# Kernel tuning notes

Hardware: AMD Instinct MI355X
Metric: run time of the kernel (lower is better)

## Reference

```python
import jax, jax.numpy as jnp
import numpy as np

NFFT = 4_194_304
NMODES = 2
NTAPS = 101
GAMMA = 0.0016567  # [/W/m]
DZ = 80000.0       # [m]


def setup_inputs() -> dict:
    key = jax.random.key(0)
    k1, k2, k3 = jax.random.split(key, 3)
    xr = jax.random.normal(k1, (NFFT, NMODES), dtype=jnp.float32)
    xi = jax.random.normal(k2, (NFFT, NMODES), dtype=jnp.float32)
    # fconv1d kernel: [ntaps, in_features=Nmodes, out_features=Nmodes] (lecun_normal-ish scale)
    W = jax.random.normal(k3, (NTAPS, NMODES, NMODES), dtype=jnp.float32) / np.sqrt(NTAPS * NMODES)
    b = jnp.zeros((NMODES,), dtype=jnp.float32)
    power = jnp.zeros((1,), dtype=jnp.float32)  # 0 dBm
    return {"xr": xr, "xi": xi, "W": W, "b": b, "power": power}


def reference(xr, xi, W, b, power):
    # P = |x|^2, shape [Nfft, Nmodes]
    P = xr * xr + xi * xi
    # valid 1D conv over time: [Nfft, Nmodes] -> [Nfft - ntaps + 1, Nmodes]
    phi = jax.lax.conv_general_dilated(
        P[None],            # [1, Nfft, Nmodes]
        W,                  # [ntaps, in, out]
        window_strides=(1,),
        padding='VALID',
        dimension_numbers=('NWC', 'WIO', 'NWC'),
    )[0] + b                # [Nfft - ntaps + 1, Nmodes]

    nmodes = xr.shape[-1]
    scale = 0.001 * 10.0 ** (power[0] / 10.0) / nmodes  # dBm -> W, per mode
    n0 = NTAPS // 2
    x = (xr + 1j * xi)[n0:xr.shape[0] - n0]  # valid-conv aligned slice
    y = x * jnp.exp(-1j * phi * (GAMMA * scale * DZ))
    return y
```

## Files before the change

### kernel.cpp

```cpp
#include <hip/hip_runtime.h>
#include <hip/hip_bf16.h>

#define NFFT   4194304
#define NMODES 2
#define NTAPS  101
#define NVALID (NFFT - NTAPS + 1)
#define N0     (NTAPS / 2)

constexpr int BLOCK = 256;
constexpr int CPT   = 8;
constexpr int TILE  = BLOCK * CPT;
constexpr int WIN   = TILE + NTAPS - 1;
constexpr int PITCH = 269;

static __device__ __forceinline__ unsigned short f2bf(float x) {
    __hip_bfloat16 h = __float2bfloat16(x);
    return *reinterpret_cast<unsigned short*>(&h);
}
static __device__ __forceinline__ unsigned pk(float e0, float e1) {
    return (unsigned)f2bf(e0) | ((unsigned)f2bf(e1) << 16);
}

__global__ __launch_bounds__(BLOCK, 4) void nl_kernel(
    const float* __restrict__ xa,
    const float* __restrict__ xb,
    const float* __restrict__ W,  const float* __restrict__ b,
    const float* __restrict__ power, unsigned* __restrict__ out)
{
    __shared__ float2 Pl[CPT * PITCH];

    const int tid = threadIdx.x;
    const int tile_start = blockIdx.x * TILE;

    const float2* __restrict__ xa2 = reinterpret_cast<const float2*>(xa);
    const float2* __restrict__ xb2 = reinterpret_cast<const float2*>(xb);
    for (int idx = tid; idx < WIN; idx += BLOCK) {
        const int g = tile_start + idx;
        float2 p = make_float2(0.f, 0.f);
        if (g < NFFT) {
            const float2 a = xa2[g];
            const float2 c = xb2[g];
            p.x = a.x * a.x + c.x * c.x;
            p.y = a.y * a.y + c.y * c.y;
        }
        Pl[(idx & 7) * PITCH + (idx >> 3)] = p;
    }
    __syncthreads();

    float acc[CPT][2];
    const float b0 = b[0], b1 = b[1];
    #pragma unroll
    for (int c = 0; c < CPT; ++c) { acc[c][0] = b0; acc[c][1] = b1; }

    const float4* __restrict__ W4 = reinterpret_cast<const float4*>(W);

    float2 w[16];
    #pragma unroll
    for (int m = 0; m < 15; ++m)
        w[m] = Pl[(m & 7) * PITCH + tid + (m >> 3)];

    for (int K = 0; K < 6; ++K) {
        const int krow = tid + 2 * K;
        #pragma unroll
        for (int j = 0; j < 16; ++j) {
            w[(j + 15) & 15] = Pl[((j + 7) & 7) * PITCH + krow + ((j + 15) >> 3)];
            const float4 wt = W4[16 * K + j];
            #pragma unroll
            for (int c = 0; c < CPT; ++c) {
                const float2 p = w[(j + c) & 15];
                acc[c][0] = fmaf(p.x, wt.x, fmaf(p.y, wt.z, acc[c][0]));
                acc[c][1] = fmaf(p.x, wt.y, fmaf(p.y, wt.w, acc[c][1]));
            }
        }
    }
    #pragma unroll
    for (int j = 0; j < 5; ++j) {
        const float4 wt = W4[96 + j];
        #pragma unroll
        for (int c = 0; c < CPT; ++c) {
            const float2 p = w[(96 + j + c) & 15];
            acc[c][0] = fmaf(p.x, wt.x, fmaf(p.y, wt.z, acc[c][0]));
            acc[c][1] = fmaf(p.x, wt.y, fmaf(p.y, wt.w, acc[c][1]));
        }
    }

    const float coef = 0.066268f * exp10f(power[0] * 0.1f);
    const int base = tile_start + tid * CPT;

    const float4* __restrict__ xa4 = reinterpret_cast<const float4*>(xa);
    const float4* __restrict__ xb4 = reinterpret_cast<const float4*>(xb);
    uint4* __restrict__ out4 = reinterpret_cast<uint4*>(out);

    #pragma unroll
    for (int cc = 0; cc < 4; ++cc) {
        const int n0 = base + 2 * cc;
        const int c0 = 2 * cc;
        if (n0 + 1 < NVALID) {
            const float4 A = xa4[(n0 + N0) >> 1];
            const float4 B = xb4[(n0 + N0) >> 1];
            float s00, c00, s01, c01, s10, c10, s11, c11;
            __sincosf(acc[c0][0]     * coef, &s00, &c00);
            __sincosf(acc[c0][1]     * coef, &s01, &c01);
            __sincosf(acc[c0 + 1][0] * coef, &s10, &c10);
            __sincosf(acc[c0 + 1][1] * coef, &s11, &c11);
            uint4 o;
            o.x = pk(B.x * c00 - A.x * s00, A.x * c00 + B.x * s00);
            o.y = pk(B.y * c01 - A.y * s01, A.y * c01 + B.y * s01);
            o.z = pk(B.z * c10 - A.z * s10, A.z * c10 + B.z * s10);
            o.w = pk(B.w * c11 - A.w * s11, A.w * c11 + B.w * s11);
            out4[n0 >> 1] = o;
        } else {
            #pragma unroll
            for (int dc = 0; dc < 2; ++dc) {
                const int n = n0 + dc;
                if (n < NVALID) {
                    const float2 A = xa2[n + N0];
                    const float2 B = xb2[n + N0];
                    float s0, c0s, s1, c1s;
                    __sincosf(acc[c0 + dc][0] * coef, &s0, &c0s);
                    __sincosf(acc[c0 + dc][1] * coef, &s1, &c1s);
                    uint2 o;
                    o.x = pk(B.x * c0s - A.x * s0, A.x * c0s + B.x * s0);
                    o.y = pk(B.y * c1s - A.y * s1, A.y * c1s + B.y * s1);
                    reinterpret_cast<uint2*>(out)[n] = o;
                }
            }
        }
    }
}

extern "C" void kernel_launch(void* const* d_in, const int* in_sizes, int n_in,
                              void* d_out, int out_size, void* d_ws, size_t ws_size,
                              hipStream_t stream) {
    const float* big[2] = {nullptr, nullptr};
    const float* W = nullptr; const float* b = nullptr; const float* power = nullptr;
    int nbig = 0;
    for (int i = 0; i < n_in; ++i) {
        const float* p = (const float*)d_in[i];
        const int sz = in_sizes[i];
        if (sz == NFFT * NMODES)       { if (nbig < 2) big[nbig++] = p; }
        else if (sz == NTAPS * NMODES * NMODES) { W = p; }
        else if (sz == NMODES)         { b = p; }
        else if (sz == 1)              { power = p; }
    }

    unsigned* out = (unsigned*)d_out;
    const int grid = (NVALID + TILE - 1) / TILE;
    nl_kernel<<<grid, BLOCK, 0, stream>>>(big[0], big[1], W, b, power, out);
}
```

Before: 137.5 us.

## Compute 101-tap convolution with bf16 MFMA using Toeplitz weight fragments in a persistent grid

```diff
diff --git a/kernel.cpp b/kernel.cpp
--- a/kernel.cpp
+++ b/kernel.cpp
@@ -8,10 +8,14 @@
 #define N0     (NTAPS / 2)
 
 constexpr int BLOCK = 256;
-constexpr int CPT   = 8;
-constexpr int TILE  = BLOCK * CPT;
-constexpr int WIN   = TILE + NTAPS - 1;
-constexpr int PITCH = 269;
+constexpr int TILE  = 2048;
+constexpr int NT    = (NVALID + TILE - 1) / TILE;
+constexpr int GRID  = 1024;
+constexpr int WIN   = 2176;
+constexpr int NM    = 15;
+
+typedef __attribute__((ext_vector_type(8)))  short short8;
+typedef __attribute__((ext_vector_type(16))) float float16;
 
 static __device__ __forceinline__ unsigned short f2bf(float x) {
     __hip_bfloat16 h = __float2bfloat16(x);
@@ -20,110 +24,101 @@
 static __device__ __forceinline__ unsigned pk(float e0, float e1) {
     return (unsigned)f2bf(e0) | ((unsigned)f2bf(e1) << 16);
 }
+static __device__ __forceinline__ int swz(int s) {
+    return s ^ (((s >> 5) & 7) << 2);
+}
 
-__global__ __launch_bounds__(BLOCK, 4) void nl_kernel(
+__global__ __launch_bounds__(BLOCK, 3) void nl_kernel(
     const float* __restrict__ xa,
     const float* __restrict__ xb,
     const float* __restrict__ W,  const float* __restrict__ b,
     const float* __restrict__ power, unsigned* __restrict__ out)
 {
-    __shared__ float2 Pl[CPT * PITCH];
+    __shared__ __align__(16) unsigned Pl[WIN];
 
-    const int tid = threadIdx.x;
-    const int tile_start = blockIdx.x * TILE;
+    const int tid  = threadIdx.x;
+    const int lane = tid & 63;
+    const int wid  = tid >> 6;
+    const int colc = lane & 31;
+    const int h    = lane >> 5;
+    const int cs   = colc >> 1;
+    const int o    = colc & 1;
+    const int r    = colc;
 
-    const float2* __restrict__ xa2 = reinterpret_cast<const float2*>(xa);
-    const float2* __restrict__ xb2 = reinterpret_cast<const float2*>(xb);
-    for (int idx = tid; idx < WIN; idx += BLOCK) {
-        const int g = tile_start + idx;
-        float2 p = make_float2(0.f, 0.f);
-        if (g < NFFT) {
-            const float2 a = xa2[g];
-            const float2 c = xb2[g];
-            p.x = a.x * a.x + c.x * c.x;
-            p.y = a.y * a.y + c.y * c.y;
+    short8 Bf[NM];
+    const float4* __restrict__ Wt = reinterpret_cast<const float4*>(W);
+    #pragma unroll
+    for (int m = 0; m < NM; ++m) {
+        short8 bb;
+        #pragma unroll
+        for (int d = 0; d < 4; ++d) {
+            const int t  = 8 * m + 4 * h + d - cs;
+            const bool ok = (unsigned)t <= 100u;
+            const float4 w = Wt[ok ? t : 0];
+            const float v0 = ok ? (o ? w.y : w.x) : 0.f;
+            const float v1 = ok ? (o ? w.w : w.z) : 0.f;
+            bb[2 * d]     = (short)f2bf(v0);
+            bb[2 * d + 1] = (short)f2bf(v1);
         }
-        Pl[(idx & 7) * PITCH + (idx >> 3)] = p;
-    }
-    __syncthreads();
-
-    float acc[CPT][2];
-    const float b0 = b[0], b1 = b[1];
-    #pragma unroll
-    for (int c = 0; c < CPT; ++c) { acc[c][0] = b0; acc[c][1] = b1; }
-
-    const float4* __restrict__ W4 = reinterpret_cast<const float4*>(W);
-
-    float2 w[16];
-    #pragma unroll
-    for (int m = 0; m < 15; ++m)
-        w[m] = Pl[(m & 7) * PITCH + tid + (m >> 3)];
-
-    for (int K = 0; K < 6; ++K) {
-        const int krow = tid + 2 * K;
-        #pragma unroll
-        for (int j = 0; j < 16; ++j) {
-            w[(j + 15) & 15] = Pl[((j + 7) & 7) * PITCH + krow + ((j + 15) >> 3)];
-            const float4 wt = W4[16 * K + j];
-            #pragma unroll
-            for (int c = 0; c < CPT; ++c) {
-                const float2 p = w[(j + c) & 15];
-                acc[c][0] = fmaf(p.x, wt.x, fmaf(p.y, wt.z, acc[c][0]));
-                acc[c][1] = fmaf(p.x, wt.y, fmaf(p.y, wt.w, acc[c][1]));
-            }
-        }
-    }
-    #pragma unroll
-    for (int j = 0; j < 5; ++j) {
-        const float4 wt = W4[96 + j];
-        #pragma unroll
-        for (int c = 0; c < CPT; ++c) {
-            const float2 p = w[(96 + j + c) & 15];
-            acc[c][0] = fmaf(p.x, wt.x, fmaf(p.y, wt.z, acc[c][0]));
-            acc[c][1] = fmaf(p.x, wt.y, fmaf(p.y, wt.w, acc[c][1]));
-        }
+        Bf[m] = bb;
     }
 
+    const float bo   = o ? b[1] : b[0];
     const float coef = 0.066268f * exp10f(power[0] * 0.1f);
-    const int base = tile_start + tid * CPT;
 
     const float4* __restrict__ xa4 = reinterpret_cast<const float4*>(xa);
     const float4* __restrict__ xb4 = reinterpret_cast<const float4*>(xb);
-    uint4* __restrict__ out4 = reinterpret_cast<uint4*>(out);
 
-    #pragma unroll
-    for (int cc = 0; cc < 4; ++cc) {
-        const int n0 = base + 2 * cc;
-        const int c0 = 2 * cc;
-        if (n0 + 1 < NVALID) {
-            const float4 A = xa4[(n0 + N0) >> 1];
-            const float4 B = xb4[(n0 + N0) >> 1];
-            float s00, c00, s01, c01, s10, c10, s11, c11;
-            __sincosf(acc[c0][0]     * coef, &s00, &c00);
-            __sincosf(acc[c0][1]     * coef, &s01, &c01);
-            __sincosf(acc[c0 + 1][0] * coef, &s10, &c10);
-            __sincosf(acc[c0 + 1][1] * coef, &s11, &c11);
-            uint4 o;
-            o.x = pk(B.x * c00 - A.x * s00, A.x * c00 + B.x * s00);
-            o.y = pk(B.y * c01 - A.y * s01, A.y * c01 + B.y * s01);
-            o.z = pk(B.z * c10 - A.z * s10, A.z * c10 + B.z * s10);
-            o.w = pk(B.w * c11 - A.w * s11, A.w * c11 + B.w * s11);
-            out4[n0 >> 1] = o;
-        } else {
-            #pragma unroll
-            for (int dc = 0; dc < 2; ++dc) {
-                const int n = n0 + dc;
-                if (n < NVALID) {
-                    const float2 A = xa2[n + N0];
-                    const float2 B = xb2[n + N0];
-                    float s0, c0s, s1, c1s;
-                    __sincosf(acc[c0 + dc][0] * coef, &s0, &c0s);
-                    __sincosf(acc[c0 + dc][1] * coef, &s1, &c1s);
-                    uint2 o;
-                    o.x = pk(B.x * c0s - A.x * s0, A.x * c0s + B.x * s0);
-                    o.y = pk(B.y * c1s - A.y * s1, A.y * c1s + B.y * s1);
-                    reinterpret_cast<uint2*>(out)[n] = o;
-                }
+    for (int tile = blockIdx.x; tile < NT; tile += GRID) {
+        const int tile_start = tile * TILE;
+        if (tile != (int)blockIdx.x) __syncthreads();
+
+        float4 sa[5], sc[5];
+        #pragma unroll
+        for (int k = 0; k < 5; ++k) {
+            const int s = 2 * tid + 512 * k;
+            const int g = tile_start + s;
+            const bool v = (k < 4 || s < WIN) && (g < NFFT);
+            sa[k] = v ? xa4[g >> 1] : make_float4(0.f, 0.f, 0.f, 0.f);
+            sc[k] = v ? xb4[g >> 1] : make_float4(0.f, 0.f, 0.f, 0.f);
+        }
+        #pragma unroll
+        for (int k = 0; k < 5; ++k) {
+            const int s = 2 * tid + 512 * k;
+            if (k < 4 || s < WIN) {
+                const float4 a = sa[k], c = sc[k];
+                const unsigned u0 = pk(a.x * a.x + c.x * c.x, a.y * a.y + c.y * c.y);
+                const unsigned u1 = pk(a.z * a.z + c.z * c.z, a.w * a.w + c.w * c.w);
+                *reinterpret_cast<uint2*>(&Pl[swz(s)]) = make_uint2(u0, u1);
+            }
+        }
+        __syncthreads();
+
+        const int cb = wid * 512;
+        float16 acc = {};
+        uint4 areg[4];
+        #pragma unroll
+        for (int m = 0; m < 4; ++m)
+            areg[m] = *reinterpret_cast<const uint4*>(&Pl[swz(cb + 16 * r + 8 * m + 4 * h)]);
+        #pragma unroll
+        for (int m = 0; m < NM; ++m) {
+            acc = __builtin_amdgcn_mfma_f32_32x32x16_bf16(
+                      __builtin_bit_cast(short8, areg[m & 3]), Bf[m], acc, 0, 0, 0);
+            if (m + 4 < NM)
+                areg[m & 3] = *reinterpret_cast<const uint4*>(
+                                  &Pl[swz(cb + 16 * r + 8 * (m + 4) + 4 * h)]);
+        }
+
+        #pragma unroll
+        for (int j = 0; j < 16; ++j) {
+            const int row = (j & 3) + 8 * (j >> 2) + 4 * h;
+            const int n   = tile_start + cb + 16 * row + cs;
+            if (n < NVALID) {
+                const float Ax = xa[(n + N0) * 2 + o];
+                const float Bx = xb[(n + N0) * 2 + o];
+                float sn, cn;
+                __sincosf((acc[j] + bo) * coef, &sn, &cn);
+                out[n * 2 + o] = pk(Bx * cn - Ax * sn, Ax * cn + Bx * sn);
             }
         }
     }
@@ -145,6 +140,5 @@
     }
 
     unsigned* out = (unsigned*)d_out;
-    const int grid = (NVALID + TILE - 1) / TILE;
-    nl_kernel<<<grid, BLOCK, 0, stream>>>(big[0], big[1], W, b, power, out);
+    nl_kernel<<<GRID, BLOCK, 0, stream>>>(big[0], big[1], W, b, power, out);
 }
```

After: 204.9 us. 1.49x slower.
